# Kernel tuning notes

Measured on AMD Instinct MI355X. Metric: run time of the kernel, lower is better.

The kernel has to match this reference:

```python
import jax, jax.numpy as jnp
import numpy as np

H = 8  # heads

def setup_inputs() -> dict:
    key = jax.random.key(0)
    k0, k1, k2, k3 = jax.random.split(key, 4)
    B, L, D = 4, 1024, 512
    K = jax.random.normal(k0, (B, L, D), dtype=jnp.float32)
    Q = jax.random.normal(k1, (B, L, D), dtype=jnp.float32)
    V = jax.random.normal(k2, (B, L, D), dtype=jnp.float32)
    # realistic padding: each doc has a valid length in [L/2, L]
    lengths = jax.random.randint(k3, (B,), L // 2, L + 1)
    pos = jnp.arange(L)
    valid = pos[None, :] < lengths[:, None]          # [B, L]
    pad_mask = valid[:, :, None] & valid[:, None, :]  # [B, L, L]
    bx_packed = ~valid                                # [B, L] True where padded
    doc_sizes = lengths.astype(jnp.float32)[:, None]  # [B, 1]
    gamma = jnp.ones((H,), dtype=jnp.float32)   # LayerNorm(heads) weight
    beta = jnp.zeros((H,), dtype=jnp.float32)   # LayerNorm(heads) bias
    return {"K": K, "Q": Q, "V": V, "doc_sizes": doc_sizes,
            "gamma": gamma, "beta": beta,
            "pad_mask": pad_mask, "bx_packed": bx_packed}


def reference(K, Q, V, doc_sizes, gamma, beta, pad_mask, bx_packed):
    B, L, D = K.shape
    d = D // H
    split = lambda x: x.reshape(B, L, H, d).transpose(0, 2, 1, 3)  # [B,H,L,d]
    k, q, v = split(K), split(Q), split(V)

    # InnerMatrix: inner-product similarity -> [B,H,L,L]
    cw = jnp.einsum('bhld,bhmd->bhlm', k, q)

    # LayerNorm over heads axis (torch views [B,H,L*L] -> [B,L*L,H], LN over H)
    mu = cw.mean(axis=1, keepdims=True)
    var = cw.var(axis=1, keepdims=True)
    cw = (cw - mu) / jnp.sqrt(var + 1e-5)
    cw = cw * gamma[None, :, None, None] + beta[None, :, None, None]
    # leaky = -1.0 default: float(leaky > 0) == 0, leaky-relu branch is a no-op

    # masked softmax over keys, NaN (fully-masked rows) -> 0
    cw = jnp.where(pad_mask[:, None, :, :], cw, -jnp.inf)
    cw = jax.nn.softmax(cw, axis=-1)
    cw = jnp.where(jnp.isnan(cw), 0.0, cw)

    # aggregated per-token weights: sum over queries, mean over heads -> [B,L]
    w = cw.sum(axis=-2).mean(axis=1)
    w = w / doc_sizes
    w = jnp.where(bx_packed, -jnp.inf, w)
    w = jax.nn.softmax(w, axis=-1)
    w = jnp.where(jnp.isnan(w), 0.0, w)

    # weighted V aggregation, merge heads back -> [B,L,D]
    out = jnp.einsum('bhlm,bhmd->bhld', cw, v)
    out = out.transpose(0, 2, 1, 3).reshape(B, L, D)
    return out, w[..., None]
```

## Files before the change

### kernel.cpp

```cpp
#include <hip/hip_runtime.h>
#include <math.h>

#define L_ 1024
#define D_ 512

typedef _Float16 half8 __attribute__((ext_vector_type(8)));
typedef _Float16 half4v __attribute__((ext_vector_type(4)));
typedef _Float16 half2v __attribute__((ext_vector_type(2)));
typedef float floatx4 __attribute__((ext_vector_type(4)));

#define LDS_PITCH 264

__global__ __launch_bounds__(256) void prep(
    const float* __restrict__ K, const float* __restrict__ Q,
    const float* __restrict__ V,
    _Float16* __restrict__ K16, _Float16* __restrict__ Q16,
    _Float16* __restrict__ Vt)
{
    __shared__ _Float16 tile[64][72];
    const int t = threadIdx.x;
    const int bi = blockIdx.x;
    if (bi < 2048) {
        #pragma unroll
        for (int it = 0; it < 2; ++it) {
            size_t f = (size_t)bi * 512 + it * 256 + t;
            const float4* src; _Float16* dst;
            if (f < 524288) { src = (const float4*)K; dst = K16; }
            else            { src = (const float4*)Q; dst = Q16; f -= 524288; }
            float4 v = src[f];
            half4v h = { (_Float16)v.x, (_Float16)v.y, (_Float16)v.z, (_Float16)v.w };
            *(half4v*)&dst[f * 4] = h;
        }
    } else {
        const int id = bi - 2048;
        const int mt = id & 15, h = (id >> 4) & 7, b = id >> 7;
        const float4* Vf4 = (const float4*)V;
        for (int it = 0; it < 4; ++it) {
            const int ml = (t >> 4) + 16 * it;
            const int c4 = t & 15;
            float4 v = Vf4[(size_t)(b * 1024 + mt * 64 + ml) * 128 + h * 16 + c4];
            tile[c4 * 4 + 0][ml] = (_Float16)v.x;
            tile[c4 * 4 + 1][ml] = (_Float16)v.y;
            tile[c4 * 4 + 2][ml] = (_Float16)v.z;
            tile[c4 * 4 + 3][ml] = (_Float16)v.w;
        }
        __syncthreads();
        const int d = t >> 2, seg = t & 3;
        half8 o0 = *(half8*)&tile[d][seg * 16];
        half8 o1 = *(half8*)&tile[d][seg * 16 + 8];
        size_t obase = ((size_t)(b * 8 + h) * 64 + d) * 1024 + mt * 64 + seg * 16;
        *(half8*)&Vt[obase] = o0;
        *(half8*)&Vt[obase + 8] = o1;
    }
}

__global__ __launch_bounds__(256) void qk_ln(
    const _Float16* __restrict__ K16, const _Float16* __restrict__ Q16,
    const float* __restrict__ gamma, const float* __restrict__ beta,
    const float* __restrict__ doc,
    _Float16* __restrict__ S, float* __restrict__ spart)
{
    __shared__ _Float16 se[8 * 16 * LDS_PITCH];

    const int t  = threadIdx.x;
    const int bi = blockIdx.x;
    const int b  = bi & 3;
    const int lt = (bi >> 2) & 63;
    const int q  = bi >> 8;
    const int wv = t >> 6, lane = t & 63;
    const int col = lane & 15, quad = lane >> 4;
    const int len = (int)doc[b];
    const int lbase = lt * 16;

    float g[8], be[8], M = 0.f;
    #pragma unroll
    for (int h = 0; h < 8; ++h) {
        g[h] = gamma[h]; be[h] = beta[h];
        M = fmaxf(M, 2.8285f * fabsf(g[h]) + fabsf(be[h]));
    }

    const _Float16* Kb = K16 + (size_t)b * 524288;
    const _Float16* Qb = Q16 + (size_t)b * 524288;
    const size_t krow = (size_t)(lbase + col) * 512;

    half8 a0[8], a1[8];
    #pragma unroll
    for (int h = 0; h < 8; ++h) {
        a0[h] = *(const half8*)&Kb[krow + h * 64 + quad * 8];
        a1[h] = *(const half8*)&Kb[krow + h * 64 + 32 + quad * 8];
    }

    float sum[8][4];
    #pragma unroll
    for (int h = 0; h < 8; ++h)
        #pragma unroll
        for (int r = 0; r < 4; ++r) sum[h][r] = 0.f;

    for (int mt = 0; mt < 4; ++mt) {
        const int m0 = q * 256 + wv * 64 + mt * 16;
        const size_t qrow = (size_t)(m0 + col) * 512;
        floatx4 c[8];
        #pragma unroll
        for (int h = 0; h < 8; ++h) {
            half8 b0 = *(const half8*)&Qb[qrow + h * 64 + quad * 8];
            half8 b1 = *(const half8*)&Qb[qrow + h * 64 + 32 + quad * 8];
            floatx4 z = {0.f, 0.f, 0.f, 0.f};
            z    = __builtin_amdgcn_mfma_f32_16x16x32_f16(a0[h], b0, z, 0, 0, 0);
            c[h] = __builtin_amdgcn_mfma_f32_16x16x32_f16(a1[h], b1, z, 0, 0, 0);
        }
        const bool mok = (m0 + col) < len;
        #pragma unroll
        for (int r = 0; r < 4; ++r) {
            const int l = lbase + quad * 4 + r;
            float mu = 0.f;
            #pragma unroll
            for (int h = 0; h < 8; ++h) mu += c[h][r];
            mu *= 0.125f;
            float var = 0.f;
            #pragma unroll
            for (int h = 0; h < 8; ++h) { float dd = c[h][r] - mu; var += dd * dd; }
            var *= 0.125f;
            const float rs = 1.0f / sqrtf(var + 1e-5f);
            const bool keep = mok && (l < len);
            #pragma unroll
            for (int h = 0; h < 8; ++h) {
                float e = 0.f;
                if (keep) {
                    float val = (c[h][r] - mu) * rs * g[h] + be[h];
                    e = __expf(val - M);
                }
                sum[h][r] += e;
                se[(h * 16 + quad * 4 + r) * LDS_PITCH + wv * 64 + mt * 16 + col] =
                    (_Float16)e;
            }
        }
    }

    #pragma unroll
    for (int h = 0; h < 8; ++h)
        #pragma unroll
        for (int r = 0; r < 4; ++r) {
            float s = sum[h][r];
            s += __shfl_xor(s, 1); s += __shfl_xor(s, 2);
            s += __shfl_xor(s, 4); s += __shfl_xor(s, 8);
            sum[h][r] = s;
        }
    if (col == 0) {
        #pragma unroll
        for (int h = 0; h < 8; ++h)
            #pragma unroll
            for (int r = 0; r < 4; ++r)
                spart[((size_t)((b * 8 + h) * 1024 + lbase + quad * 4 + r)) * 16
                      + q * 4 + wv] = sum[h][r];
    }
    __syncthreads();

    for (int it = 0; it < 16; ++it) {
        const int rr = it * 8 + (t >> 5);
        const int h = rr >> 4, l = rr & 15;
        half8 v = *(half8*)&se[rr * LDS_PITCH + (t & 31) * 8];
        *(half8*)&S[((size_t)((b * 8 + h) * 1024 + lbase + l)) * 1024
                    + q * 256 + (t & 31) * 8] = v;
    }
}

__global__ __launch_bounds__(512) void pv(
    const _Float16* __restrict__ S, const _Float16* __restrict__ Vt,
    const float* __restrict__ spart, const float* __restrict__ doc,
    float* __restrict__ out)
{
    __shared__ float inv_s[64];
    __shared__ float comb[4][64][20];

    const int t = threadIdx.x, wv = t >> 6, lane = t & 63;
    const int col = lane & 15, quad = lane >> 4;
    const int bi = blockIdx.x;
    const int lb = bi & 15, h = (bi >> 4) & 7, b = bi >> 7;
    const int lg = wv & 3, mh = wv >> 2;
    const int l0 = lb * 64 + lg * 16;
    const size_t rbase = (size_t)(b * 8 + h) * 1024 + lb * 64;

    if (t < 64) {
        const int len = (int)doc[b];
        float s = 0.f;
        #pragma unroll
        for (int j = 0; j < 16; ++j) s += spart[(rbase + t) * 16 + j];
        inv_s[t] = ((lb * 64 + t) < len && s > 0.f) ? 1.0f / s : 0.f;
    }

    const _Float16* Arow = S + ((size_t)(b * 8 + h) * 1024 + l0 + col) * 1024
                         + mh * 512;
    const _Float16* Vb = Vt + (size_t)(b * 8 + h) * 65536 + (size_t)col * 1024
                       + quad * 8 + mh * 512;

    floatx4 acc[4] = {{0,0,0,0},{0,0,0,0},{0,0,0,0},{0,0,0,0}};

    half8 ebuf[8];
    #pragma unroll
    for (int i = 0; i < 8; ++i)
        ebuf[i] = *(const half8*)&Arow[i * 32 + quad * 8];

    half8 va[4], vb[4];
    #pragma unroll
    for (int dt = 0; dt < 4; ++dt)
        va[dt] = *(const half8*)&Vb[(size_t)(dt * 16) * 1024];

    #pragma unroll
    for (int kc = 0; kc < 16; kc += 2) {
        half8 ae = ebuf[kc & 7];
        if (kc + 8 < 16)
            ebuf[kc & 7] = *(const half8*)&Arow[(kc + 8) * 32 + quad * 8];
        #pragma unroll
        for (int dt = 0; dt < 4; ++dt)
            vb[dt] = *(const half8*)&Vb[(size_t)(dt * 16) * 1024 + (kc + 1) * 32];
        #pragma unroll
        for (int dt = 0; dt < 4; ++dt)
            acc[dt] = __builtin_amdgcn_mfma_f32_16x16x32_f16(ae, va[dt], acc[dt], 0, 0, 0);

        half8 ao = ebuf[(kc + 1) & 7];
        if (kc + 9 < 16)
            ebuf[(kc + 1) & 7] = *(const half8*)&Arow[(kc + 9) * 32 + quad * 8];
        if (kc + 2 < 16) {
            #pragma unroll
            for (int dt = 0; dt < 4; ++dt)
                va[dt] = *(const half8*)&Vb[(size_t)(dt * 16) * 1024 + (kc + 2) * 32];
        }
        #pragma unroll
        for (int dt = 0; dt < 4; ++dt)
            acc[dt] = __builtin_amdgcn_mfma_f32_16x16x32_f16(ao, vb[dt], acc[dt], 0, 0, 0);
    }

    if (mh == 1) {
        #pragma unroll
        for (int dt = 0; dt < 4; ++dt)
            *(floatx4*)&comb[lg][lane][dt * 4] = acc[dt];
    }
    __syncthreads();
    if (mh == 0) {
        #pragma unroll
        for (int dt = 0; dt < 4; ++dt)
            acc[dt] += *(floatx4*)&comb[lg][lane][dt * 4];
        #pragma unroll
        for (int r = 0; r < 4; ++r) {
            const int l = l0 + quad * 4 + r;
            const float ivr = inv_s[lg * 16 + quad * 4 + r];
            float* orow = out + (size_t)(b * 1024 + l) * 512 + h * 64;
            #pragma unroll
            for (int dt = 0; dt < 4; ++dt)
                orow[dt * 16 + col] = acc[dt][r] * ivr;
        }
    }
}

__global__ __launch_bounds__(512) void wsum(
    const _Float16* __restrict__ S, const float* __restrict__ spart,
    const float* __restrict__ doc, float* __restrict__ wacc)
{
    __shared__ float inv_s[64];
    __shared__ float ws[4][1024];
    const int t = threadIdx.x;
    const int bi = blockIdx.x;
    const int lc = bi & 15, h = (bi >> 4) & 7, b = bi >> 7;
    const size_t rbase = (size_t)(b * 8 + h) * 1024 + lc * 64;

    if (t < 64) {
        const int len = (int)doc[b];
        float s = 0.f;
        #pragma unroll
        for (int j = 0; j < 16; ++j) s += spart[(rbase + t) * 16 + j];
        inv_s[t] = ((lc * 64 + t) < len && s > 0.f) ? 1.0f / s : 0.f;
    }
    __syncthreads();

    const _Float16* Sb = S + rbase * 1024;
    const int mi = (t & 127) * 8;
    const int lp = t >> 7;

    float acc[8];
    #pragma unroll
    for (int j = 0; j < 8; ++j) acc[j] = 0.f;

    #pragma unroll 4
    for (int l = lp; l < 64; l += 4) {
        const float iv = inv_s[l];
        half8 e = *(const half8*)&Sb[(size_t)l * 1024 + mi];
        #pragma unroll
        for (int j = 0; j < 8; ++j) acc[j] += (float)e[j] * iv;
    }

    #pragma unroll
    for (int j = 0; j < 8; ++j) ws[lp][mi + j] = acc[j];
    __syncthreads();

    if (t < 256) {
        float* wb = wacc + b * 1024;
        #pragma unroll
        for (int i = 0; i < 4; ++i) {
            const int m = t * 4 + i;
            atomicAdd(&wb[m], ws[0][m] + ws[1][m] + ws[2][m] + ws[3][m]);
        }
    }
}

__global__ __launch_bounds__(256) void w_final(
    const float* __restrict__ wacc, const float* __restrict__ doc,
    float* __restrict__ wout)
{
    const int b = blockIdx.x;
    const int t = threadIdx.x;
    __shared__ float red[4];

    const float ds = doc[b];
    const int len = (int)ds;

    float v[4];
    float mx = -INFINITY;
    #pragma unroll
    for (int i = 0; i < 4; ++i) {
        const int m = t + 256 * i;
        const float raw = wacc[b * L_ + m];
        v[i] = (m < len) ? (raw * 0.125f) / ds : -INFINITY;
        mx = fmaxf(mx, v[i]);
    }
    #pragma unroll
    for (int off = 1; off < 64; off <<= 1) mx = fmaxf(mx, __shfl_xor(mx, off));
    if ((t & 63) == 0) red[t >> 6] = mx;
    __syncthreads();
    mx = fmaxf(fmaxf(red[0], red[1]), fmaxf(red[2], red[3]));

    float e[4];
    float sm = 0.f;
    #pragma unroll
    for (int i = 0; i < 4; ++i) {
        e[i] = (v[i] != -INFINITY) ? __expf(v[i] - mx) : 0.f;
        sm += e[i];
    }
    #pragma unroll
    for (int off = 1; off < 64; off <<= 1) sm += __shfl_xor(sm, off);
    __syncthreads();
    if ((t & 63) == 0) red[t >> 6] = sm;
    __syncthreads();
    sm = red[0] + red[1] + red[2] + red[3];
    const float inv = (sm > 0.f) ? 1.0f / sm : 0.f;

    #pragma unroll
    for (int i = 0; i < 4; ++i)
        wout[b * L_ + t + 256 * i] = e[i] * inv;
}

extern "C" void kernel_launch(void* const* d_in, const int* in_sizes, int n_in,
                              void* d_out, int out_size, void* d_ws, size_t ws_size,
                              hipStream_t stream)
{
    const float* K     = (const float*)d_in[0];
    const float* Q     = (const float*)d_in[1];
    const float* V     = (const float*)d_in[2];
    const float* doc   = (const float*)d_in[3];
    const float* gamma = (const float*)d_in[4];
    const float* beta  = (const float*)d_in[5];

    float* out  = (float*)d_out;
    float* wout = out + (size_t)4 * L_ * D_;

    _Float16* S    = (_Float16*)d_ws;
    _Float16* K16  = S + (size_t)33554432;
    _Float16* Q16  = K16 + 2097152;
    _Float16* Vt   = Q16 + 2097152;
    float*    spart = (float*)(Vt + 2097152);
    float*    wacc  = spart + 524288 + 32768;

    hipMemsetAsync(wacc, 0, 4096 * sizeof(float), stream);
    prep   <<<dim3(2560), dim3(256), 0, stream>>>(K, Q, V, K16, Q16, Vt);
    qk_ln  <<<dim3(1024), dim3(256), 0, stream>>>(K16, Q16, gamma, beta, doc, S, spart);
    pv     <<<dim3(512),  dim3(512), 0, stream>>>(S, Vt, spart, doc, out);
    wsum   <<<dim3(512),  dim3(512), 0, stream>>>(S, spart, doc, wacc);
    w_final<<<dim3(4),    dim3(256), 0, stream>>>(wacc, doc, wout);
}
```

Baseline: 209.6 us.

## Halve qk_ln LDS staging with two head passes and merge pv/wsum launches

qk_ln now stages the exp scores in two passes of four heads each, so its LDS buffer shrinks from 128 rows to 64 rows. The intent is to raise occupancy, at the cost of recomputing the QK MFMAs and the LayerNorm statistics twice and adding extra barriers. The pv and wsum kernels are combined into one 1024-block launch that branches on block index, removing a launch gap and letting the two kinds of work overlap. The merged kernel uses one shared-memory buffer sized for the larger of the two branches.

```diff
diff --git a/kernel.cpp b/kernel.cpp
--- a/kernel.cpp
+++ b/kernel.cpp
@@ -60,7 +60,7 @@
     const float* __restrict__ doc,
     _Float16* __restrict__ S, float* __restrict__ spart)
 {
-    __shared__ _Float16 se[8 * 16 * LDS_PITCH];
+    __shared__ _Float16 se[64 * LDS_PITCH];
 
     const int t  = threadIdx.x;
     const int bi = blockIdx.x;
@@ -96,44 +96,59 @@
         #pragma unroll
         for (int r = 0; r < 4; ++r) sum[h][r] = 0.f;
 
-    for (int mt = 0; mt < 4; ++mt) {
-        const int m0 = q * 256 + wv * 64 + mt * 16;
-        const size_t qrow = (size_t)(m0 + col) * 512;
-        floatx4 c[8];
-        #pragma unroll
-        for (int h = 0; h < 8; ++h) {
-            half8 b0 = *(const half8*)&Qb[qrow + h * 64 + quad * 8];
-            half8 b1 = *(const half8*)&Qb[qrow + h * 64 + 32 + quad * 8];
-            floatx4 z = {0.f, 0.f, 0.f, 0.f};
-            z    = __builtin_amdgcn_mfma_f32_16x16x32_f16(a0[h], b0, z, 0, 0, 0);
-            c[h] = __builtin_amdgcn_mfma_f32_16x16x32_f16(a1[h], b1, z, 0, 0, 0);
-        }
-        const bool mok = (m0 + col) < len;
-        #pragma unroll
-        for (int r = 0; r < 4; ++r) {
-            const int l = lbase + quad * 4 + r;
-            float mu = 0.f;
-            #pragma unroll
-            for (int h = 0; h < 8; ++h) mu += c[h][r];
-            mu *= 0.125f;
-            float var = 0.f;
-            #pragma unroll
-            for (int h = 0; h < 8; ++h) { float dd = c[h][r] - mu; var += dd * dd; }
-            var *= 0.125f;
-            const float rs = 1.0f / sqrtf(var + 1e-5f);
-            const bool keep = mok && (l < len);
+    #pragma unroll
+    for (int pass = 0; pass < 2; ++pass) {
+        const int h0 = pass * 4;
+        for (int mt = 0; mt < 4; ++mt) {
+            const int m0 = q * 256 + wv * 64 + mt * 16;
+            const size_t qrow = (size_t)(m0 + col) * 512;
+            floatx4 c[8];
             #pragma unroll
             for (int h = 0; h < 8; ++h) {
-                float e = 0.f;
-                if (keep) {
-                    float val = (c[h][r] - mu) * rs * g[h] + be[h];
-                    e = __expf(val - M);
+                half8 b0 = *(const half8*)&Qb[qrow + h * 64 + quad * 8];
+                half8 b1 = *(const half8*)&Qb[qrow + h * 64 + 32 + quad * 8];
+                floatx4 z = {0.f, 0.f, 0.f, 0.f};
+                z    = __builtin_amdgcn_mfma_f32_16x16x32_f16(a0[h], b0, z, 0, 0, 0);
+                c[h] = __builtin_amdgcn_mfma_f32_16x16x32_f16(a1[h], b1, z, 0, 0, 0);
+            }
+            const bool mok = (m0 + col) < len;
+            #pragma unroll
+            for (int r = 0; r < 4; ++r) {
+                const int l = lbase + quad * 4 + r;
+                float mu = 0.f;
+                #pragma unroll
+                for (int h = 0; h < 8; ++h) mu += c[h][r];
+                mu *= 0.125f;
+                float var = 0.f;
+                #pragma unroll
+                for (int h = 0; h < 8; ++h) { float dd = c[h][r] - mu; var += dd * dd; }
+                var *= 0.125f;
+                const float rs = 1.0f / sqrtf(var + 1e-5f);
+                const bool keep = mok && (l < len);
+                #pragma unroll
+                for (int hh = 0; hh < 4; ++hh) {
+                    const int h = h0 + hh;
+                    float e = 0.f;
+                    if (keep) {
+                        float val = (c[h][r] - mu) * rs * g[h] + be[h];
+                        e = __expf(val - M);
+                    }
+                    sum[h][r] += e;
+                    se[(hh * 16 + quad * 4 + r) * LDS_PITCH + wv * 64 + mt * 16 + col] =
+                        (_Float16)e;
                 }
-                sum[h][r] += e;
-                se[(h * 16 + quad * 4 + r) * LDS_PITCH + wv * 64 + mt * 16 + col] =
-                    (_Float16)e;
-            }
-        }
+            }
+        }
+        __syncthreads();
+        #pragma unroll
+        for (int it = 0; it < 8; ++it) {
+            const int rr = it * 8 + (t >> 5);
+            const int h = h0 + (rr >> 4), l = rr & 15;
+            half8 v = *(half8*)&se[rr * LDS_PITCH + (t & 31) * 8];
+            *(half8*)&S[((size_t)((b * 8 + h) * 1024 + lbase + l)) * 1024
+                        + q * 256 + (t & 31) * 8] = v;
+        }
+        __syncthreads();
     }
 
     #pragma unroll
@@ -153,151 +168,140 @@
                 spart[((size_t)((b * 8 + h) * 1024 + lbase + quad * 4 + r)) * 16
                       + q * 4 + wv] = sum[h][r];
     }
-    __syncthreads();
-
-    for (int it = 0; it < 16; ++it) {
-        const int rr = it * 8 + (t >> 5);
-        const int h = rr >> 4, l = rr & 15;
-        half8 v = *(half8*)&se[rr * LDS_PITCH + (t & 31) * 8];
-        *(half8*)&S[((size_t)((b * 8 + h) * 1024 + lbase + l)) * 1024
-                    + q * 256 + (t & 31) * 8] = v;
-    }
-}
-
-__global__ __launch_bounds__(512) void pv(
+}
+
+__global__ __launch_bounds__(512) void spv(
     const _Float16* __restrict__ S, const _Float16* __restrict__ Vt,
     const float* __restrict__ spart, const float* __restrict__ doc,
-    float* __restrict__ out)
-{
-    __shared__ float inv_s[64];
-    __shared__ float comb[4][64][20];
-
-    const int t = threadIdx.x, wv = t >> 6, lane = t & 63;
-    const int col = lane & 15, quad = lane >> 4;
-    const int bi = blockIdx.x;
-    const int lb = bi & 15, h = (bi >> 4) & 7, b = bi >> 7;
-    const int lg = wv & 3, mh = wv >> 2;
-    const int l0 = lb * 64 + lg * 16;
-    const size_t rbase = (size_t)(b * 8 + h) * 1024 + lb * 64;
-
-    if (t < 64) {
-        const int len = (int)doc[b];
-        float s = 0.f;
-        #pragma unroll
-        for (int j = 0; j < 16; ++j) s += spart[(rbase + t) * 16 + j];
-        inv_s[t] = ((lb * 64 + t) < len && s > 0.f) ? 1.0f / s : 0.f;
-    }
-
-    const _Float16* Arow = S + ((size_t)(b * 8 + h) * 1024 + l0 + col) * 1024
-                         + mh * 512;
-    const _Float16* Vb = Vt + (size_t)(b * 8 + h) * 65536 + (size_t)col * 1024
-                       + quad * 8 + mh * 512;
-
-    floatx4 acc[4] = {{0,0,0,0},{0,0,0,0},{0,0,0,0},{0,0,0,0}};
-
-    half8 ebuf[8];
-    #pragma unroll
-    for (int i = 0; i < 8; ++i)
-        ebuf[i] = *(const half8*)&Arow[i * 32 + quad * 8];
-
-    half8 va[4], vb[4];
-    #pragma unroll
-    for (int dt = 0; dt < 4; ++dt)
-        va[dt] = *(const half8*)&Vb[(size_t)(dt * 16) * 1024];
-
-    #pragma unroll
-    for (int kc = 0; kc < 16; kc += 2) {
-        half8 ae = ebuf[kc & 7];
-        if (kc + 8 < 16)
-            ebuf[kc & 7] = *(const half8*)&Arow[(kc + 8) * 32 + quad * 8];
-        #pragma unroll
-        for (int dt = 0; dt < 4; ++dt)
-            vb[dt] = *(const half8*)&Vb[(size_t)(dt * 16) * 1024 + (kc + 1) * 32];
-        #pragma unroll
-        for (int dt = 0; dt < 4; ++dt)
-            acc[dt] = __builtin_amdgcn_mfma_f32_16x16x32_f16(ae, va[dt], acc[dt], 0, 0, 0);
-
-        half8 ao = ebuf[(kc + 1) & 7];
-        if (kc + 9 < 16)
-            ebuf[(kc + 1) & 7] = *(const half8*)&Arow[(kc + 9) * 32 + quad * 8];
-        if (kc + 2 < 16) {
-            #pragma unroll
-            for (int dt = 0; dt < 4; ++dt)
-                va[dt] = *(const half8*)&Vb[(size_t)(dt * 16) * 1024 + (kc + 2) * 32];
-        }
-        #pragma unroll
-        for (int dt = 0; dt < 4; ++dt)
-            acc[dt] = __builtin_amdgcn_mfma_f32_16x16x32_f16(ao, vb[dt], acc[dt], 0, 0, 0);
-    }
-
-    if (mh == 1) {
-        #pragma unroll
-        for (int dt = 0; dt < 4; ++dt)
-            *(floatx4*)&comb[lg][lane][dt * 4] = acc[dt];
-    }
-    __syncthreads();
-    if (mh == 0) {
-        #pragma unroll
-        for (int dt = 0; dt < 4; ++dt)
-            acc[dt] += *(floatx4*)&comb[lg][lane][dt * 4];
-        #pragma unroll
-        for (int r = 0; r < 4; ++r) {
-            const int l = l0 + quad * 4 + r;
-            const float ivr = inv_s[lg * 16 + quad * 4 + r];
-            float* orow = out + (size_t)(b * 1024 + l) * 512 + h * 64;
-            #pragma unroll
-            for (int dt = 0; dt < 4; ++dt)
-                orow[dt * 16 + col] = acc[dt][r] * ivr;
-        }
-    }
-}
-
-__global__ __launch_bounds__(512) void wsum(
-    const _Float16* __restrict__ S, const float* __restrict__ spart,
-    const float* __restrict__ doc, float* __restrict__ wacc)
-{
-    __shared__ float inv_s[64];
-    __shared__ float ws[4][1024];
+    float* __restrict__ out, float* __restrict__ wacc)
+{
+    __shared__ float smem[5248];
     const int t = threadIdx.x;
     const int bi = blockIdx.x;
-    const int lc = bi & 15, h = (bi >> 4) & 7, b = bi >> 7;
-    const size_t rbase = (size_t)(b * 8 + h) * 1024 + lc * 64;
-
-    if (t < 64) {
-        const int len = (int)doc[b];
-        float s = 0.f;
-        #pragma unroll
-        for (int j = 0; j < 16; ++j) s += spart[(rbase + t) * 16 + j];
-        inv_s[t] = ((lc * 64 + t) < len && s > 0.f) ? 1.0f / s : 0.f;
-    }
-    __syncthreads();
-
-    const _Float16* Sb = S + rbase * 1024;
-    const int mi = (t & 127) * 8;
-    const int lp = t >> 7;
-
-    float acc[8];
-    #pragma unroll
-    for (int j = 0; j < 8; ++j) acc[j] = 0.f;
-
-    #pragma unroll 4
-    for (int l = lp; l < 64; l += 4) {
-        const float iv = inv_s[l];
-        half8 e = *(const half8*)&Sb[(size_t)l * 1024 + mi];
-        #pragma unroll
-        for (int j = 0; j < 8; ++j) acc[j] += (float)e[j] * iv;
-    }
-
-    #pragma unroll
-    for (int j = 0; j < 8; ++j) ws[lp][mi + j] = acc[j];
-    __syncthreads();
-
-    if (t < 256) {
-        float* wb = wacc + b * 1024;
-        #pragma unroll
-        for (int i = 0; i < 4; ++i) {
-            const int m = t * 4 + i;
-            atomicAdd(&wb[m], ws[0][m] + ws[1][m] + ws[2][m] + ws[3][m]);
+
+    if (bi < 512) {
+        float* inv_s = smem;
+        float* comb = smem + 64;
+        const int wv = t >> 6, lane = t & 63;
+        const int col = lane & 15, quad = lane >> 4;
+        const int lb = bi & 15, h = (bi >> 4) & 7, b = bi >> 7;
+        const int lg = wv & 3, mh = wv >> 2;
+        const int l0 = lb * 64 + lg * 16;
+        const size_t rbase = (size_t)(b * 8 + h) * 1024 + lb * 64;
+
+        if (t < 64) {
+            const int len = (int)doc[b];
+            float s = 0.f;
+            #pragma unroll
+            for (int j = 0; j < 16; ++j) s += spart[(rbase + t) * 16 + j];
+            inv_s[t] = ((lb * 64 + t) < len && s > 0.f) ? 1.0f / s : 0.f;
+        }
+
+        const _Float16* Arow = S + ((size_t)(b * 8 + h) * 1024 + l0 + col) * 1024
+                             + mh * 512;
+        const _Float16* Vb = Vt + (size_t)(b * 8 + h) * 65536 + (size_t)col * 1024
+                           + quad * 8 + mh * 512;
+
+        floatx4 acc[4] = {{0,0,0,0},{0,0,0,0},{0,0,0,0},{0,0,0,0}};
+
+        half8 ebuf[8];
+        #pragma unroll
+        for (int i = 0; i < 8; ++i)
+            ebuf[i] = *(const half8*)&Arow[i * 32 + quad * 8];
+
+        half8 va[4], vb[4];
+        #pragma unroll
+        for (int dt = 0; dt < 4; ++dt)
+            va[dt] = *(const half8*)&Vb[(size_t)(dt * 16) * 1024];
+
+        #pragma unroll
+        for (int kc = 0; kc < 16; kc += 2) {
+            half8 ae = ebuf[kc & 7];
+            if (kc + 8 < 16)
+                ebuf[kc & 7] = *(const half8*)&Arow[(kc + 8) * 32 + quad * 8];
+            #pragma unroll
+            for (int dt = 0; dt < 4; ++dt)
+                vb[dt] = *(const half8*)&Vb[(size_t)(dt * 16) * 1024 + (kc + 1) * 32];
+            #pragma unroll
+            for (int dt = 0; dt < 4; ++dt)
+                acc[dt] = __builtin_amdgcn_mfma_f32_16x16x32_f16(ae, va[dt], acc[dt], 0, 0, 0);
+
+            half8 ao = ebuf[(kc + 1) & 7];
+            if (kc + 9 < 16)
+                ebuf[(kc + 1) & 7] = *(const half8*)&Arow[(kc + 9) * 32 + quad * 8];
+            if (kc + 2 < 16) {
+                #pragma unroll
+                for (int dt = 0; dt < 4; ++dt)
+                    va[dt] = *(const half8*)&Vb[(size_t)(dt * 16) * 1024 + (kc + 2) * 32];
+            }
+            #pragma unroll
+            for (int dt = 0; dt < 4; ++dt)
+                acc[dt] = __builtin_amdgcn_mfma_f32_16x16x32_f16(ao, vb[dt], acc[dt], 0, 0, 0);
+        }
+
+        if (mh == 1) {
+            #pragma unroll
+            for (int dt = 0; dt < 4; ++dt)
+                *(floatx4*)&comb[(lg * 64 + lane) * 20 + dt * 4] = acc[dt];
+        }
+        __syncthreads();
+        if (mh == 0) {
+            #pragma unroll
+            for (int dt = 0; dt < 4; ++dt)
+                acc[dt] += *(floatx4*)&comb[(lg * 64 + lane) * 20 + dt * 4];
+            #pragma unroll
+            for (int r = 0; r < 4; ++r) {
+                const int l = l0 + quad * 4 + r;
+                const float ivr = inv_s[lg * 16 + quad * 4 + r];
+                float* orow = out + (size_t)(b * 1024 + l) * 512 + h * 64;
+                #pragma unroll
+                for (int dt = 0; dt < 4; ++dt)
+                    orow[dt * 16 + col] = acc[dt][r] * ivr;
+            }
+        }
+    } else {
+        float* inv_s = smem;
+        float* ws = smem + 64;
+        const int bj = bi - 512;
+        const int lc = bj & 15, h = (bj >> 4) & 7, b = bj >> 7;
+        const size_t rbase = (size_t)(b * 8 + h) * 1024 + lc * 64;
+
+        if (t < 64) {
+            const int len = (int)doc[b];
+            float s = 0.f;
+            #pragma unroll
+            for (int j = 0; j < 16; ++j) s += spart[(rbase + t) * 16 + j];
+            inv_s[t] = ((lc * 64 + t) < len && s > 0.f) ? 1.0f / s : 0.f;
+        }
+        __syncthreads();
+
+        const _Float16* Sb = S + rbase * 1024;
+        const int mi = (t & 127) * 8;
+        const int lp = t >> 7;
+
+        float acc[8];
+        #pragma unroll
+        for (int j = 0; j < 8; ++j) acc[j] = 0.f;
+
+        #pragma unroll 4
+        for (int l = lp; l < 64; l += 4) {
+            const float iv = inv_s[l];
+            half8 e = *(const half8*)&Sb[(size_t)l * 1024 + mi];
+            #pragma unroll
+            for (int j = 0; j < 8; ++j) acc[j] += (float)e[j] * iv;
+        }
+
+        #pragma unroll
+        for (int j = 0; j < 8; ++j) ws[lp * 1024 + mi + j] = acc[j];
+        __syncthreads();
+
+        if (t < 256) {
+            float* wb = wacc + b * 1024;
+            #pragma unroll
+            for (int i = 0; i < 4; ++i) {
+                const int m = t * 4 + i;
+                atomicAdd(&wb[m], ws[m] + ws[1024 + m] + ws[2048 + m] + ws[3072 + m]);
+            }
         }
     }
 }
@@ -372,7 +376,6 @@
     hipMemsetAsync(wacc, 0, 4096 * sizeof(float), stream);
     prep   <<<dim3(2560), dim3(256), 0, stream>>>(K, Q, V, K16, Q16, Vt);
     qk_ln  <<<dim3(1024), dim3(256), 0, stream>>>(K16, Q16, gamma, beta, doc, S, spart);
-    pv     <<<dim3(512),  dim3(512), 0, stream>>>(S, Vt, spart, doc, out);
-    wsum   <<<dim3(512),  dim3(512), 0, stream>>>(S, spart, doc, wacc);
+    spv    <<<dim3(1024), dim3(512), 0, stream>>>(S, Vt, spart, doc, out, wacc);
     w_final<<<dim3(4),    dim3(256), 0, stream>>>(wacc, doc, wout);
 }
```

Measured after the change: 265.2 us. +26.5%, slower.

## Fuse per-token weight column sums into PV kernel and drop wsum pass

Applied to the files above, without the earlier changes.

Removes the separate wsum kernel, which re-read the whole fp16 score matrix S. The PV kernel now scales each S tile by the row inverse sum before the MFMA and builds the column sums with wave shuffles, LDS atomics and one global atomic per column. The prep kernel also gets fewer, larger blocks for the K/Q conversion. In exchange the PV inner loop gains extra VALU work, cross-lane shuffles and LDS atomics, and the column sums now run in fp16, which can cost accuracy.

```diff
diff --git a/kernel.cpp b/kernel.cpp
--- a/kernel.cpp
+++ b/kernel.cpp
@@ -20,10 +20,9 @@
     __shared__ _Float16 tile[64][72];
     const int t = threadIdx.x;
     const int bi = blockIdx.x;
-    if (bi < 2048) {
-        #pragma unroll
-        for (int it = 0; it < 2; ++it) {
-            size_t f = (size_t)bi * 512 + it * 256 + t;
+    if (bi < 256) {
+        for (int it = 0; it < 16; ++it) {
+            size_t f = (size_t)bi * 4096 + it * 256 + t;
             const float4* src; _Float16* dst;
             if (f < 524288) { src = (const float4*)K; dst = K16; }
             else            { src = (const float4*)Q; dst = Q16; f -= 524288; }
@@ -32,7 +31,7 @@
             *(half4v*)&dst[f * 4] = h;
         }
     } else {
-        const int id = bi - 2048;
+        const int id = bi - 256;
         const int mt = id & 15, h = (id >> 4) & 7, b = id >> 7;
         const float4* Vf4 = (const float4*)V;
         for (int it = 0; it < 4; ++it) {
@@ -167,9 +166,10 @@
 __global__ __launch_bounds__(512) void pv(
     const _Float16* __restrict__ S, const _Float16* __restrict__ Vt,
     const float* __restrict__ spart, const float* __restrict__ doc,
-    float* __restrict__ out)
+    float* __restrict__ out, float* __restrict__ wacc)
 {
     __shared__ float inv_s[64];
+    __shared__ float cs[1024];
     __shared__ float comb[4][64][20];
 
     const int t = threadIdx.x, wv = t >> 6, lane = t & 63;
@@ -180,6 +180,7 @@
     const int l0 = lb * 64 + lg * 16;
     const size_t rbase = (size_t)(b * 8 + h) * 1024 + lb * 64;
 
+    cs[t] = 0.f; cs[t + 512] = 0.f;
     if (t < 64) {
         const int len = (int)doc[b];
         float s = 0.f;
@@ -187,6 +188,9 @@
         for (int j = 0; j < 16; ++j) s += spart[(rbase + t) * 16 + j];
         inv_s[t] = ((lb * 64 + t) < len && s > 0.f) ? 1.0f / s : 0.f;
     }
+    __syncthreads();
+
+    const float inv = inv_s[lg * 16 + col];
 
     const _Float16* Arow = S + ((size_t)(b * 8 + h) * 1024 + l0 + col) * 1024
                          + mh * 512;
@@ -200,24 +204,49 @@
     for (int i = 0; i < 8; ++i)
         ebuf[i] = *(const half8*)&Arow[i * 32 + quad * 8];
 
-    half8 va[4], vb[4];
+    half8 va[4], vb2[4];
     #pragma unroll
     for (int dt = 0; dt < 4; ++dt)
         va[dt] = *(const half8*)&Vb[(size_t)(dt * 16) * 1024];
 
     #pragma unroll
     for (int kc = 0; kc < 16; kc += 2) {
-        half8 ae = ebuf[kc & 7];
+        half8 e0 = ebuf[kc & 7];
         if (kc + 8 < 16)
             ebuf[kc & 7] = *(const half8*)&Arow[(kc + 8) * 32 + quad * 8];
         #pragma unroll
         for (int dt = 0; dt < 4; ++dt)
-            vb[dt] = *(const half8*)&Vb[(size_t)(dt * 16) * 1024 + (kc + 1) * 32];
-        #pragma unroll
-        for (int dt = 0; dt < 4; ++dt)
-            acc[dt] = __builtin_amdgcn_mfma_f32_16x16x32_f16(ae, va[dt], acc[dt], 0, 0, 0);
-
-        half8 ao = ebuf[(kc + 1) & 7];
+            vb2[dt] = *(const half8*)&Vb[(size_t)(dt * 16) * 1024 + (kc + 1) * 32];
+
+        half8 a;
+        #pragma unroll
+        for (int j = 0; j < 8; ++j) a[j] = (_Float16)((float)e0[j] * inv);
+        {
+            const int mbase = mh * 512 + kc * 32 + quad * 8;
+            #pragma unroll
+            for (int u = 0; u < 4; ++u) {
+                half2v p2 = { a[2 * u], a[2 * u + 1] };
+                int bits = *(int*)&p2;
+                #pragma unroll
+                for (int o = 1; o < 16; o <<= 1) {
+                    int ob = __shfl_xor(bits, o);
+                    half2v po = *(half2v*)&ob;
+                    half2v pc = *(half2v*)&bits;
+                    pc[0] = pc[0] + po[0]; pc[1] = pc[1] + po[1];
+                    bits = *(int*)&pc;
+                }
+                if (col == 0) {
+                    half2v pc = *(half2v*)&bits;
+                    atomicAdd(&cs[mbase + 2 * u],     (float)pc[0]);
+                    atomicAdd(&cs[mbase + 2 * u + 1], (float)pc[1]);
+                }
+            }
+        }
+        #pragma unroll
+        for (int dt = 0; dt < 4; ++dt)
+            acc[dt] = __builtin_amdgcn_mfma_f32_16x16x32_f16(a, va[dt], acc[dt], 0, 0, 0);
+
+        half8 e1 = ebuf[(kc + 1) & 7];
         if (kc + 9 < 16)
             ebuf[(kc + 1) & 7] = *(const half8*)&Arow[(kc + 9) * 32 + quad * 8];
         if (kc + 2 < 16) {
@@ -225,9 +254,34 @@
             for (int dt = 0; dt < 4; ++dt)
                 va[dt] = *(const half8*)&Vb[(size_t)(dt * 16) * 1024 + (kc + 2) * 32];
         }
-        #pragma unroll
-        for (int dt = 0; dt < 4; ++dt)
-            acc[dt] = __builtin_amdgcn_mfma_f32_16x16x32_f16(ao, vb[dt], acc[dt], 0, 0, 0);
+
+        half8 a2;
+        #pragma unroll
+        for (int j = 0; j < 8; ++j) a2[j] = (_Float16)((float)e1[j] * inv);
+        {
+            const int mbase = mh * 512 + (kc + 1) * 32 + quad * 8;
+            #pragma unroll
+            for (int u = 0; u < 4; ++u) {
+                half2v p2 = { a2[2 * u], a2[2 * u + 1] };
+                int bits = *(int*)&p2;
+                #pragma unroll
+                for (int o = 1; o < 16; o <<= 1) {
+                    int ob = __shfl_xor(bits, o);
+                    half2v po = *(half2v*)&ob;
+                    half2v pc = *(half2v*)&bits;
+                    pc[0] = pc[0] + po[0]; pc[1] = pc[1] + po[1];
+                    bits = *(int*)&pc;
+                }
+                if (col == 0) {
+                    half2v pc = *(half2v*)&bits;
+                    atomicAdd(&cs[mbase + 2 * u],     (float)pc[0]);
+                    atomicAdd(&cs[mbase + 2 * u + 1], (float)pc[1]);
+                }
+            }
+        }
+        #pragma unroll
+        for (int dt = 0; dt < 4; ++dt)
+            acc[dt] = __builtin_amdgcn_mfma_f32_16x16x32_f16(a2, vb2[dt], acc[dt], 0, 0, 0);
     }
 
     if (mh == 1) {
@@ -243,63 +297,14 @@
         #pragma unroll
         for (int r = 0; r < 4; ++r) {
             const int l = l0 + quad * 4 + r;
-            const float ivr = inv_s[lg * 16 + quad * 4 + r];
             float* orow = out + (size_t)(b * 1024 + l) * 512 + h * 64;
             #pragma unroll
             for (int dt = 0; dt < 4; ++dt)
-                orow[dt * 16 + col] = acc[dt][r] * ivr;
-        }
-    }
-}
-
-__global__ __launch_bounds__(512) void wsum(
-    const _Float16* __restrict__ S, const float* __restrict__ spart,
-    const float* __restrict__ doc, float* __restrict__ wacc)
-{
-    __shared__ float inv_s[64];
-    __shared__ float ws[4][1024];
-    const int t = threadIdx.x;
-    const int bi = blockIdx.x;
-    const int lc = bi & 15, h = (bi >> 4) & 7, b = bi >> 7;
-    const size_t rbase = (size_t)(b * 8 + h) * 1024 + lc * 64;
-
-    if (t < 64) {
-        const int len = (int)doc[b];
-        float s = 0.f;
-        #pragma unroll
-        for (int j = 0; j < 16; ++j) s += spart[(rbase + t) * 16 + j];
-        inv_s[t] = ((lc * 64 + t) < len && s > 0.f) ? 1.0f / s : 0.f;
-    }
-    __syncthreads();
-
-    const _Float16* Sb = S + rbase * 1024;
-    const int mi = (t & 127) * 8;
-    const int lp = t >> 7;
-
-    float acc[8];
-    #pragma unroll
-    for (int j = 0; j < 8; ++j) acc[j] = 0.f;
-
-    #pragma unroll 4
-    for (int l = lp; l < 64; l += 4) {
-        const float iv = inv_s[l];
-        half8 e = *(const half8*)&Sb[(size_t)l * 1024 + mi];
-        #pragma unroll
-        for (int j = 0; j < 8; ++j) acc[j] += (float)e[j] * iv;
-    }
-
-    #pragma unroll
-    for (int j = 0; j < 8; ++j) ws[lp][mi + j] = acc[j];
-    __syncthreads();
-
-    if (t < 256) {
-        float* wb = wacc + b * 1024;
-        #pragma unroll
-        for (int i = 0; i < 4; ++i) {
-            const int m = t * 4 + i;
-            atomicAdd(&wb[m], ws[0][m] + ws[1][m] + ws[2][m] + ws[3][m]);
-        }
-    }
+                orow[dt * 16 + col] = acc[dt][r];
+        }
+    }
+    atomicAdd(&wacc[b * 1024 + t],       cs[t]);
+    atomicAdd(&wacc[b * 1024 + t + 512], cs[t + 512]);
 }
 
 __global__ __launch_bounds__(256) void w_final(
@@ -370,9 +375,8 @@
     float*    wacc  = spart + 524288 + 32768;
 
     hipMemsetAsync(wacc, 0, 4096 * sizeof(float), stream);
-    prep   <<<dim3(2560), dim3(256), 0, stream>>>(K, Q, V, K16, Q16, Vt);
+    prep   <<<dim3(768),  dim3(256), 0, stream>>>(K, Q, V, K16, Q16, Vt);
     qk_ln  <<<dim3(1024), dim3(256), 0, stream>>>(K16, Q16, gamma, beta, doc, S, spart);
-    pv     <<<dim3(512),  dim3(512), 0, stream>>>(S, Vt, spart, doc, out);
-    wsum   <<<dim3(512),  dim3(512), 0, stream>>>(S, spart, doc, wacc);
+    pv     <<<dim3(512),  dim3(512), 0, stream>>>(S, Vt, spart, doc, out, wacc);
     w_final<<<dim3(4),    dim3(256), 0, stream>>>(wacc, doc, wout);
 }
```

New measurement: 190.7 us. -9.0%, faster.
